# Optimization experiments

Hardware: AMD Instinct MI355X
Metric: run time of the kernel (lower is better)

The kernel has to match this reference:

```python
import jax, jax.numpy as jnp
import numpy as np

H = 16
D_MODEL = 1024
D_K = D_MODEL // H
MAX_REL = 16
REL_VOCAB = 2 * MAX_REL + 1


def _rel_pos_ids(seq_len):
    r = jnp.arange(seq_len)
    dist = r[None, :] - r[:, None]                      # [S,S]
    return jnp.clip(dist, -MAX_REL, MAX_REL) + MAX_REL  # in [0, 2*MAX_REL]


def setup_inputs() -> dict:
    key = jax.random.key(0)
    ks = jax.random.split(key, 16)
    B, S = 2, 2048
    f32 = jnp.float32
    inp = {
        "query": jax.random.normal(ks[0], (B, S, D_MODEL), f32),
        "key": jax.random.normal(ks[1], (B, S, D_MODEL), f32),
        "value": jax.random.normal(ks[2], (B, S, D_MODEL), f32),
        # four nn.Linear(d_model, d_model): W [out,in], b [out]
        "Wq": jax.random.normal(ks[3], (D_MODEL, D_MODEL), f32) * 0.02,
        "bq": jnp.zeros((D_MODEL,), f32),
        "Wk": jax.random.normal(ks[4], (D_MODEL, D_MODEL), f32) * 0.02,
        "bk": jnp.zeros((D_MODEL,), f32),
        "Wv": jax.random.normal(ks[5], (D_MODEL, D_MODEL), f32) * 0.02,
        "bv": jnp.zeros((D_MODEL,), f32),
        "Wo": jax.random.normal(ks[6], (D_MODEL, D_MODEL), f32) * 0.02,
        "bo": jnp.zeros((D_MODEL,), f32),
        # relative-position embedding tables (keys and values)
        "rel_k_table": jax.random.normal(ks[7], (REL_VOCAB, D_K), f32) * 0.02,
        "rel_v_table": jax.random.normal(ks[8], (REL_VOCAB, D_K), f32) * 0.02,
    }
    return inp


def reference(query, key, value, Wq, bq, Wk, bk, Wv, bv, Wo, bo,
              rel_k_table, rel_v_table):
    B, S, E = query.shape
    ids = _rel_pos_ids(S)                    # [S,S] int
    rel_k = rel_k_table[ids]                 # [S,S,d_k]
    rel_v = rel_v_table[ids]                 # [S,S,d_k]

    def proj(x, W, b):
        y = x @ W.T + b                      # [B,S,E]
        return y.reshape(B, S, H, D_K).transpose(0, 2, 1, 3)  # [B,H,S,d_k]

    q = proj(query, Wq, bq)
    k = proj(key, Wk, bk)
    v = proj(value, Wv, bv)

    # NOTE: original has no 1/sqrt(d_k) scaling and ignores mask — faithful.
    logits = jnp.einsum('bhqd,bhkd->bhqk', q, k) \
           + jnp.einsum('bhqd,qkd->bhqk', q, rel_k)
    w = jax.nn.softmax(logits, axis=-1)      # [B,H,S,S]

    x = jnp.einsum('bhqk,bhkd->bhqd', w, v) \
      + jnp.einsum('bhqk,qkd->bhqd', w, rel_v)

    x = x.transpose(0, 2, 1, 3).reshape(B, S, H * D_K)
    return x @ Wo.T + bo
```

## Files before the change

kernel.cpp:

```cpp
#include <hip/hip_runtime.h>
#include <hip/hip_bf16.h>

typedef unsigned short u16;
typedef __attribute__((ext_vector_type(8))) short short8;
typedef __attribute__((ext_vector_type(4))) short short4_t;
typedef __attribute__((ext_vector_type(4))) float f32x4;

#define MFMA16(a, b, c) __builtin_amdgcn_mfma_f32_16x16x32_bf16((a), (b), (c), 0, 0, 0)

#if __has_builtin(__builtin_amdgcn_mfma_f32_16x16x16bf16_1k)
#define MFMAK16(a, b, c) __builtin_amdgcn_mfma_f32_16x16x16bf16_1k((a), (b), (c), 0, 0, 0)
#elif __has_builtin(__builtin_amdgcn_mfma_f32_16x16x16_bf16)
#define MFMAK16(a, b, c) __builtin_amdgcn_mfma_f32_16x16x16_bf16((a), (b), (c), 0, 0, 0)
#else
__device__ __forceinline__ f32x4 mfmak16_asm(short4_t a, short4_t b, f32x4 c) {
  asm("v_mfma_f32_16x16x16_bf16 %0, %1, %2, %0" : "+v"(c) : "v"(a), "v"(b));
  return c;
}
#define MFMAK16(a, b, c) mfmak16_asm((a), (b), (c))
#endif

#define GLOAD_LDS16(gp, lp)                                          \
  __builtin_amdgcn_global_load_lds(                                  \
      (const __attribute__((address_space(1))) void*)(gp),           \
      (__attribute__((address_space(3))) void*)(lp), 16, 0, 0)
#define SBAR() asm volatile("s_barrier" ::: "memory")
#define WAIT_LGKM0() asm volatile("s_waitcnt lgkmcnt(0)" ::: "memory")
#define WAIT_VM0() asm volatile("s_waitcnt vmcnt(0)" ::: "memory")

__device__ __forceinline__ float us2f(u16 u) {
  union { unsigned int i; float f; } c; c.i = ((unsigned int)u) << 16; return c.f;
}
__device__ __forceinline__ u16 f2us(float f) {
  union { float f; unsigned int i; } c; c.f = f;
  return (u16)((c.i + 0x7fffu + ((c.i >> 16) & 1u)) >> 16);
}
__device__ __forceinline__ unsigned int f2us2(float a, float b) {
  union { __hip_bfloat162 h; unsigned int u; } c;
  c.h = __float22bfloat162_rn(float2{a, b});
  return c.u;
}

__global__ __launch_bounds__(256) void cvt_all_kernel(
    const float* x0, const float* x1, const float* x2, const float* w0,
    const float* w1, const float* w2, const float* w3, u16* y0, u16* y1,
    u16* y2, u16* z0, u16* z1, u16* z2, u16* z3) {
  const int z = blockIdx.z;
  const float* src; u16* dst; int n;
  switch (z) {
    case 0: src = x0; dst = y0; n = 4194304; break;
    case 1: src = x1; dst = y1; n = 4194304; break;
    case 2: src = x2; dst = y2; n = 4194304; break;
    case 3: src = w0; dst = z0; n = 1048576; break;
    case 4: src = w1; dst = z1; n = 1048576; break;
    case 5: src = w2; dst = z2; n = 1048576; break;
    default: src = w3; dst = z3; n = 1048576; break;
  }
  const int i = (blockIdx.x * 256 + threadIdx.x) * 8;
  if (i < n) {
    const float4 a = *(const float4*)(src + i);
    const float4 b = *(const float4*)(src + i + 4);
    unsigned int o[4];
    o[0] = f2us2(a.x, a.y); o[1] = f2us2(a.z, a.w);
    o[2] = f2us2(b.x, b.y); o[3] = f2us2(b.z, b.w);
    *(uint4*)(dst + i) = *(uint4*)o;
  }
}

__global__ __launch_bounds__(256) void cvt_relk_kernel(const float* relk, u16* relkb) {
  const int i = blockIdx.x * 256 + threadIdx.x;
  if (i < 4096) relkb[i] = (i < 2112) ? f2us(relk[i]) : (u16)0;
}

template <int MODE, typename OUT>
__device__ __forceinline__ void gemm_body(u16* __restrict__ SM,
                                          const u16* __restrict__ X,
                                          const u16* __restrict__ W,
                                          const float* __restrict__ bias,
                                          OUT* __restrict__ Y, int row0, int col0) {
  u16* As = SM;
  u16* Bs = SM + 8192;
  const int tid = threadIdx.x;
  const int lane = tid & 63;
  const int wid = tid >> 6;
  const int wm = wid >> 1, wn = wid & 1;
  const int l15 = lane & 15, l16 = lane >> 4;
  const int lrow = lane >> 3;
  const int lchunk = (lane & 7) ^ lrow;

  f32x4 acc[4][4];
#pragma unroll
  for (int i = 0; i < 4; i++)
#pragma unroll
    for (int j = 0; j < 4; j++) acc[i][j] = (f32x4){0.f, 0.f, 0.f, 0.f};

  for (int k0 = 0; k0 < 1024; k0 += 64) {
#pragma unroll
    for (int i = 0; i < 4; i++) {
      const int rb = wid * 32 + i * 8;
      GLOAD_LDS16(X + (size_t)(row0 + rb + lrow) * 1024 + k0 + lchunk * 8, &As[rb * 64]);
      GLOAD_LDS16(W + (size_t)(col0 + rb + lrow) * 1024 + k0 + lchunk * 8, &Bs[rb * 64]);
    }
    __syncthreads();
#pragma unroll
    for (int kk = 0; kk < 2; kk++) {
      const int ch = kk * 4 + l16;
      short8 af[4], bfr[4];
#pragma unroll
      for (int t = 0; t < 4; t++) {
        const int m = wm * 64 + t * 16 + l15;
        af[t] = *(const short8*)&As[m * 64 + ((ch ^ (m & 7)) * 8)];
        const int n = wn * 64 + t * 16 + l15;
        bfr[t] = *(const short8*)&Bs[n * 64 + ((ch ^ (n & 7)) * 8)];
      }
#pragma unroll
      for (int tm = 0; tm < 4; tm++)
#pragma unroll
        for (int tn = 0; tn < 4; tn++)
          acc[tm][tn] = MFMA16(af[tm], bfr[tn], acc[tm][tn]);
    }
    __syncthreads();
  }

  if (MODE == 0) {
#pragma unroll
    for (int tn = 0; tn < 4; tn++) {
      const int col = col0 + wn * 64 + tn * 16 + l15;
      const float bv = bias[col];
#pragma unroll
      for (int tm = 0; tm < 4; tm++) {
        const int rowb = row0 + wm * 64 + tm * 16 + l16 * 4;
#pragma unroll
        for (int r = 0; r < 4; r++)
          Y[(size_t)(rowb + r) * 1024 + col] = (OUT)(acc[tm][tn][r] + bv);
      }
    }
  } else {
    u16* T = SM;
    const int bb = row0 >> 11;
    const int sbase = row0 & 2047;
#pragma unroll
    for (int pass = 0; pass < 2; pass++) {
      __syncthreads();
      if (wm == pass) {
#pragma unroll
        for (int tn = 0; tn < 4; tn++) {
          const int coll = wn * 64 + tn * 16 + l15;
          const float bv = bias[col0 + coll];
#pragma unroll
          for (int tm = 0; tm < 4; tm++) {
            if (MODE == 1) {
#pragma unroll
              for (int r = 0; r < 4; r++)
                T[(tm * 16 + l16 * 4 + r) * 136 + coll] = f2us(acc[tm][tn][r] + bv);
            } else {
              unsigned int o[2];
              o[0] = f2us2(acc[tm][tn][0] + bv, acc[tm][tn][1] + bv);
              o[1] = f2us2(acc[tm][tn][2] + bv, acc[tm][tn][3] + bv);
              *(short4_t*)&T[coll * 72 + tm * 16 + l16 * 4] = *(short4_t*)o;
            }
          }
        }
      }
      __syncthreads();
      if (MODE == 1) {
#pragma unroll
        for (int i = 0; i < 8; i++) {
          const int idx = tid + i * 256;
          const int srow = idx >> 5, c4 = idx & 31;
          const short4_t v = *(const short4_t*)&T[srow * 136 + c4 * 4];
          const int col = col0 + c4 * 4;
          const int hh = col >> 6, dd = col & 63;
          const int s = sbase + pass * 64 + srow;
          *(short4_t*)&((u16*)Y)[(((size_t)(bb * 16 + hh)) * 2048 + s) * 64 + dd] = v;
        }
      } else {
#pragma unroll
        for (int i = 0; i < 4; i++) {
          const int idx = tid + i * 256;
          const int cl = idx >> 3, sc = idx & 7;
          const short8 v = *(const short8*)&T[cl * 72 + sc * 8];
          const int col = col0 + cl;
          const int hh = col >> 6, dd = col & 63;
          const int s = sbase + pass * 64 + sc * 8;
          *(short8*)&((u16*)Y)[(((size_t)(bb * 16 + hh)) * 64 + dd) * 2048 + s] = v;
        }
      }
    }
  }
}

__global__ __launch_bounds__(256) void qkv_kernel(
    const u16* Xq, const u16* Xk, const u16* Xv, const u16* Wq, const u16* Wk,
    const u16* Wv, const float* bq, const float* bk, const float* bv, u16* Yq,
    u16* Yk, u16* Yv) {
  __shared__ __align__(16) u16 SM[16384];
  const int z = blockIdx.z;
  const u16* X = z == 0 ? Xq : (z == 1 ? Xk : Xv);
  const u16* W = z == 0 ? Wq : (z == 1 ? Wk : Wv);
  const float* bi = z == 0 ? bq : (z == 1 ? bk : bv);
  u16* Y = z == 0 ? Yq : (z == 1 ? Yk : Yv);
  if (z == 2)
    gemm_body<2, u16>(SM, X, W, bi, Y, blockIdx.x * 128, blockIdx.y * 128);
  else
    gemm_body<1, u16>(SM, X, W, bi, Y, blockIdx.x * 128, blockIdx.y * 128);
}

__global__ __launch_bounds__(256) void oproj_kernel(const u16* Xc, const u16* Wo,
                                                    const float* bo, float* out) {
  __shared__ __align__(16) u16 SM[16384];
  gemm_body<0, float>(SM, Xc, Wo, bo, out, blockIdx.x * 128, blockIdx.y * 128);
}

__global__ __launch_bounds__(256, 6) void attn_kernel(
    const u16* __restrict__ Qg, const u16* __restrict__ Kg,
    const u16* __restrict__ Vtg, const u16* __restrict__ relkb,
    const float* __restrict__ relv, u16* __restrict__ ctx) {
  __shared__ __align__(16) u16 KV[8192];
  __shared__ __align__(16) u16 qrelJ[64 * 33];
  __shared__ __align__(16) u16 wsum[64 * 31];

  const int tid = threadIdx.x, lane = tid & 63, wid = tid >> 6;
  const int l15 = lane & 15, l16 = lane >> 4;
  const int bh = blockIdx.x;
  const int b = bh >> 4, h = bh & 15;
  const int q0 = blockIdx.y * 64;
  const u16* Qb = Qg + (size_t)bh * 2048 * 64;
  const u16* Kb = Kg + (size_t)bh * 2048 * 64;
  const u16* Vtb = Vtg + (size_t)bh * 64 * 2048;

  const int lrow = lane >> 3;
  const int lchunk = (lane & 7) ^ lrow;
  const int qw = wid * 16;
  const int kq4 = l16 * 4;
  const int qrow = qw + l15;

#pragma unroll
  for (int i = 0; i < 2; i++) {
    const int rb = wid * 16 + i * 8;
    GLOAD_LDS16(Qb + (size_t)(q0 + rb + lrow) * 64 + lchunk * 8, &KV[rb * 64]);
  }
  for (int idx = tid; idx < 992; idx += 256) ((unsigned int*)wsum)[idx] = 0u;
  __syncthreads();

  short8 aq[2];
  {
    const int m = qw + l15;
    aq[0] = *(const short8*)&KV[m * 64 + ((l16 ^ (m & 7)) * 8)];
    aq[1] = *(const short8*)&KV[m * 64 + (((4 + l16) ^ (m & 7)) * 8)];
  }
  {
    f32x4 qa[3];
#pragma unroll
    for (int nt = 0; nt < 3; nt++) {
      qa[nt] = (f32x4){0.f, 0.f, 0.f, 0.f};
#pragma unroll
      for (int kk = 0; kk < 2; kk++) {
        const short8 bf =
            *(const short8*)(relkb + (nt * 16 + l15) * 64 + kk * 32 + l16 * 8);
        qa[nt] = MFMA16(aq[kk], bf, qa[nt]);
      }
    }
#pragma unroll
    for (int nt = 0; nt < 3; nt++) {
      if (nt < 2 || l15 == 0) {
#pragma unroll
        for (int r = 0; r < 4; r++)
          qrelJ[(qw + kq4 + r) * 33 + nt * 16 + l15] = f2us(qa[nt][r]);
      }
    }
  }
  WAIT_LGKM0();
  const float q0r = us2f(qrelJ[qrow * 33 + 0]);
  const float q32r = us2f(qrelJ[qrow * 33 + 32]);

  float l_acc = 0.f, wl_acc = 0.f, wr_acc = 0.f;
  f32x4 Oacc[4];
#pragma unroll
  for (int t = 0; t < 4; t++) Oacc[t] = (f32x4){0.f, 0.f, 0.f, 0.f};

  for (int kt = 0; kt < 32; kt++) {
    SBAR();
    const int k0 = kt * 64;
#pragma unroll
    for (int i = 0; i < 2; i++) {
      const int rb = wid * 16 + i * 8;
      GLOAD_LDS16(Kb + (size_t)(k0 + rb + lrow) * 64 + lchunk * 8, &KV[rb * 64]);
    }
#pragma unroll
    for (int i = 0; i < 2; i++) {
      const int rb = wid * 16 + i * 8;
      GLOAD_LDS16(Vtb + (size_t)(rb + lrow) * 2048 + k0 + lchunk * 8,
                  &KV[4096 + rb * 64]);
    }
    WAIT_VM0();
    SBAR();

    short4_t pf[4];
    if (k0 + 79 <= q0 || k0 >= q0 + 79) {
      const float eb = (k0 < q0) ? q0r : q32r;
      float ts = 0.f;
#pragma unroll
      for (int tn = 0; tn < 4; tn++) {
        f32x4 sac = (f32x4){0.f, 0.f, 0.f, 0.f};
#pragma unroll
        for (int kk = 0; kk < 2; kk++) {
          const int n = tn * 16 + l15;
          const short8 bk = *(const short8*)&KV[n * 64 + (((kk * 4 + l16) ^ (n & 7)) * 8)];
          sac = MFMA16(bk, aq[kk], sac);
        }
        float p0 = __expf(sac[0] + eb), p1 = __expf(sac[1] + eb);
        float p2 = __expf(sac[2] + eb), p3 = __expf(sac[3] + eb);
        ts += (p0 + p1) + (p2 + p3);
        union { unsigned int u[2]; short4_t s; } c;
        c.u[0] = f2us2(p0, p1);
        c.u[1] = f2us2(p2, p3);
        pf[tn] = c.s;
      }
      l_acc += ts;
      if (k0 < q0) wl_acc += ts; else wr_acc += ts;
    } else {
#pragma unroll
      for (int tn = 0; tn < 4; tn++) {
        f32x4 sac = (f32x4){0.f, 0.f, 0.f, 0.f};
#pragma unroll
        for (int kk = 0; kk < 2; kk++) {
          const int n = tn * 16 + l15;
          const short8 bk = *(const short8*)&KV[n * 64 + (((kk * 4 + l16) ^ (n & 7)) * 8)];
          sac = MFMA16(bk, aq[kk], sac);
        }
        float pv4[4];
#pragma unroll
        for (int r = 0; r < 4; r++) {
          const int kg = k0 + tn * 16 + kq4 + r;
          const int dlt = kg - (q0 + qrow);
          const int jj = (dlt < -16 ? -16 : (dlt > 16 ? 16 : dlt)) + 16;
          const float pv = __expf(sac[r] + us2f(qrelJ[qrow * 33 + jj]));
          pv4[r] = pv;
          l_acc += pv;
          if (dlt <= -16) wl_acc += pv;
          else if (dlt >= 16) wr_acc += pv;
          else wsum[qrow * 31 + (dlt + 15)] = f2us(pv);
        }
        union { unsigned int u[2]; short4_t s; } c;
        c.u[0] = f2us2(pv4[0], pv4[1]);
        c.u[1] = f2us2(pv4[2], pv4[3]);
        pf[tn] = c.s;
      }
    }

#pragma unroll
    for (int td = 0; td < 4; td++) {
      const int row = td * 16 + l15;
      const int rs = row & 7;
#pragma unroll
      for (int kk = 0; kk < 4; kk++) {
        const short4_t vf = *(const short4_t*)&KV[4096 + row * 64 +
                                                  (((kk * 2 + (l16 >> 1)) ^ rs) * 8) +
                                                  (l16 & 1) * 4];
        Oacc[td] = MFMAK16(vf, pf[kk], Oacc[td]);
      }
    }
  }

  l_acc += __shfl_xor(l_acc, 16); l_acc += __shfl_xor(l_acc, 32);
  wl_acc += __shfl_xor(wl_acc, 16); wl_acc += __shfl_xor(wl_acc, 32);
  wr_acc += __shfl_xor(wr_acc, 16); wr_acc += __shfl_xor(wr_acc, 32);
  const float linv = 1.f / l_acc;
  wl_acc *= linv; wr_acc *= linv;

#pragma unroll
  for (int td = 0; td < 4; td++) {
    const f32x4 rv0 = *(const f32x4*)&relv[td * 16 + kq4];
    const f32x4 rv32 = *(const f32x4*)&relv[32 * 64 + td * 16 + kq4];
#pragma unroll
    for (int r = 0; r < 4; r++)
      Oacc[td][r] = Oacc[td][r] * linv + wl_acc * rv0[r] + wr_acc * rv32[r];
  }
  WAIT_LGKM0();
  for (int j = 1; j <= 31; j++) {
    const float wv = us2f(wsum[qrow * 31 + (j - 1)]) * linv;
#pragma unroll
    for (int td = 0; td < 4; td++) {
      const f32x4 rv = *(const f32x4*)&relv[j * 64 + td * 16 + kq4];
#pragma unroll
      for (int r = 0; r < 4; r++) Oacc[td][r] += wv * rv[r];
    }
  }
  SBAR();
#pragma unroll
  for (int td = 0; td < 4; td++) {
    unsigned int o[2];
    o[0] = f2us2(Oacc[td][0], Oacc[td][1]);
    o[1] = f2us2(Oacc[td][2], Oacc[td][3]);
    *(short4_t*)&KV[qrow * 72 + td * 16 + kq4] = *(short4_t*)o;
  }
  WAIT_LGKM0();
  SBAR();
#pragma unroll
  for (int i = 0; i < 2; i++) {
    const int idx = tid + i * 256;
    const int q = idx >> 3, sc = idx & 7;
    const short8 v = *(const short8*)&KV[q * 72 + sc * 8];
    *(short8*)&ctx[((size_t)b * 2048 + q0 + q) * 1024 + h * 64 + sc * 8] = v;
  }
}

extern "C" void kernel_launch(void* const* d_in, const int* in_sizes, int n_in,
                              void* d_out, int out_size, void* d_ws, size_t ws_size,
                              hipStream_t stream) {
  u16* qb = (u16*)d_ws;
  u16* kb = qb + 4194304;
  u16* vtb = kb + 4194304;
  u16* ctx = vtb + 4194304;
  u16* Xq = ctx + 4194304;
  u16* Xk = Xq + 4194304;
  u16* Xv = Xk + 4194304;
  u16* Wqb = Xv + 4194304;
  u16* Wkb = Wqb + 1048576;
  u16* Wvb = Wkb + 1048576;
  u16* Wob = Wvb + 1048576;
  u16* relkb = Wob + 1048576;

  const float* bq = (const float*)d_in[4];
  const float* bk = (const float*)d_in[6];
  const float* bv = (const float*)d_in[8];
  const float* bo = (const float*)d_in[10];
  const float* relk = (const float*)d_in[11];
  const float* relv = (const float*)d_in[12];

  dim3 blk(256);
  cvt_all_kernel<<<dim3(2048, 1, 7), blk, 0, stream>>>(
      (const float*)d_in[0], (const float*)d_in[1], (const float*)d_in[2],
      (const float*)d_in[3], (const float*)d_in[5], (const float*)d_in[7],
      (const float*)d_in[9], Xq, Xk, Xv, Wqb, Wkb, Wvb, Wob);
  cvt_relk_kernel<<<16, blk, 0, stream>>>(relk, relkb);
  qkv_kernel<<<dim3(32, 8, 3), blk, 0, stream>>>(Xq, Xk, Xv, Wqb, Wkb, Wvb, bq,
                                                 bk, bv, qb, kb, vtb);
  attn_kernel<<<dim3(32, 32), blk, 0, stream>>>(qb, kb, vtb, relkb, relv, ctx);
  oproj_kernel<<<dim3(32, 8), blk, 0, stream>>>(ctx, Wob, bo, (float*)d_out);
}
```

Baseline: 269.2 us.

## Double-buffer K/V tiles in attention and switch softmax to exp2

The attention kernel now double-buffers K and V^T tiles in LDS. It prefetches the next key tile with async global-to-LDS loads while computing on the current one, and uses partial vmcnt waits instead of a full drain every iteration. Q is pre-scaled by log2(e) in the QKV projection epilogue, so the softmax can use the hardware exp2 instruction; the relative-key logits are built from this scaled Q, so they stay consistent. The separate relk conversion kernel is merged into the bulk conversion kernel to save a launch, and s_setprio is raised around the PV MFMA block. In exchange, LDS use doubles and the launch-bounds occupancy hint drops from 6 to 4 blocks per CU.

```diff
diff --git a/kernel.cpp b/kernel.cpp
--- a/kernel.cpp
+++ b/kernel.cpp
@@ -27,6 +27,9 @@
 #define SBAR() asm volatile("s_barrier" ::: "memory")
 #define WAIT_LGKM0() asm volatile("s_waitcnt lgkmcnt(0)" ::: "memory")
 #define WAIT_VM0() asm volatile("s_waitcnt vmcnt(0)" ::: "memory")
+#define WAIT_VM4() asm volatile("s_waitcnt vmcnt(4)" ::: "memory")
+
+#define LOG2E 1.44269504088896340736f
 
 __device__ __forceinline__ float us2f(u16 u) {
   union { unsigned int i; float f; } c; c.i = ((unsigned int)u) << 16; return c.f;
@@ -40,12 +43,37 @@
   c.h = __float22bfloat162_rn(float2{a, b});
   return c.u;
 }
+__device__ __forceinline__ float exp2fast(float x) {
+#if __has_builtin(__builtin_amdgcn_exp2f)
+  return __builtin_amdgcn_exp2f(x);
+#else
+  return exp2f(x);
+#endif
+}
 
 __global__ __launch_bounds__(256) void cvt_all_kernel(
     const float* x0, const float* x1, const float* x2, const float* w0,
-    const float* w1, const float* w2, const float* w3, u16* y0, u16* y1,
-    u16* y2, u16* z0, u16* z1, u16* z2, u16* z3) {
+    const float* w1, const float* w2, const float* w3, const float* relk,
+    u16* y0, u16* y1, u16* y2, u16* z0, u16* z1, u16* z2, u16* z3,
+    u16* relkb) {
   const int z = blockIdx.z;
+  if (z == 7) {
+    const int i = (blockIdx.x * 256 + threadIdx.x) * 8;
+    if (i < 4096) {
+      if (i < 2112) {
+        const float4 a = *(const float4*)(relk + i);
+        const float4 b = *(const float4*)(relk + i + 4);
+        unsigned int o[4];
+        o[0] = f2us2(a.x, a.y); o[1] = f2us2(a.z, a.w);
+        o[2] = f2us2(b.x, b.y); o[3] = f2us2(b.z, b.w);
+        *(uint4*)(relkb + i) = *(uint4*)o;
+      } else {
+        uint4 zz = {0u, 0u, 0u, 0u};
+        *(uint4*)(relkb + i) = zz;
+      }
+    }
+    return;
+  }
   const float* src; u16* dst; int n;
   switch (z) {
     case 0: src = x0; dst = y0; n = 4194304; break;
@@ -67,17 +95,13 @@
   }
 }
 
-__global__ __launch_bounds__(256) void cvt_relk_kernel(const float* relk, u16* relkb) {
-  const int i = blockIdx.x * 256 + threadIdx.x;
-  if (i < 4096) relkb[i] = (i < 2112) ? f2us(relk[i]) : (u16)0;
-}
-
 template <int MODE, typename OUT>
 __device__ __forceinline__ void gemm_body(u16* __restrict__ SM,
                                           const u16* __restrict__ X,
                                           const u16* __restrict__ W,
                                           const float* __restrict__ bias,
-                                          OUT* __restrict__ Y, int row0, int col0) {
+                                          OUT* __restrict__ Y, int row0, int col0,
+                                          float oscale) {
   u16* As = SM;
   u16* Bs = SM + 8192;
   const int tid = threadIdx.x;
@@ -152,7 +176,7 @@
             if (MODE == 1) {
 #pragma unroll
               for (int r = 0; r < 4; r++)
-                T[(tm * 16 + l16 * 4 + r) * 136 + coll] = f2us(acc[tm][tn][r] + bv);
+                T[(tm * 16 + l16 * 4 + r) * 136 + coll] = f2us((acc[tm][tn][r] + bv) * oscale);
             } else {
               unsigned int o[2];
               o[0] = f2us2(acc[tm][tn][0] + bv, acc[tm][tn][1] + bv);
@@ -201,22 +225,23 @@
   const float* bi = z == 0 ? bq : (z == 1 ? bk : bv);
   u16* Y = z == 0 ? Yq : (z == 1 ? Yk : Yv);
   if (z == 2)
-    gemm_body<2, u16>(SM, X, W, bi, Y, blockIdx.x * 128, blockIdx.y * 128);
+    gemm_body<2, u16>(SM, X, W, bi, Y, blockIdx.x * 128, blockIdx.y * 128, 1.0f);
   else
-    gemm_body<1, u16>(SM, X, W, bi, Y, blockIdx.x * 128, blockIdx.y * 128);
+    gemm_body<1, u16>(SM, X, W, bi, Y, blockIdx.x * 128, blockIdx.y * 128,
+                      z == 0 ? LOG2E : 1.0f);
 }
 
 __global__ __launch_bounds__(256) void oproj_kernel(const u16* Xc, const u16* Wo,
                                                     const float* bo, float* out) {
   __shared__ __align__(16) u16 SM[16384];
-  gemm_body<0, float>(SM, Xc, Wo, bo, out, blockIdx.x * 128, blockIdx.y * 128);
-}
-
-__global__ __launch_bounds__(256, 6) void attn_kernel(
+  gemm_body<0, float>(SM, Xc, Wo, bo, out, blockIdx.x * 128, blockIdx.y * 128, 1.0f);
+}
+
+__global__ __launch_bounds__(256, 4) void attn_kernel(
     const u16* __restrict__ Qg, const u16* __restrict__ Kg,
     const u16* __restrict__ Vtg, const u16* __restrict__ relkb,
     const float* __restrict__ relv, u16* __restrict__ ctx) {
-  __shared__ __align__(16) u16 KV[8192];
+  __shared__ __align__(16) u16 KV[16384];
   __shared__ __align__(16) u16 qrelJ[64 * 33];
   __shared__ __align__(16) u16 wsum[64 * 31];
 
@@ -237,11 +262,22 @@
 
 #pragma unroll
   for (int i = 0; i < 2; i++) {
-    const int rb = wid * 16 + i * 8;
+    const int rb = qw + i * 8;
     GLOAD_LDS16(Qb + (size_t)(q0 + rb + lrow) * 64 + lchunk * 8, &KV[rb * 64]);
   }
+#pragma unroll
+  for (int i = 0; i < 2; i++) {
+    const int rb = qw + i * 8;
+    GLOAD_LDS16(Kb + (size_t)(rb + lrow) * 64 + lchunk * 8, &KV[8192 + rb * 64]);
+  }
+#pragma unroll
+  for (int i = 0; i < 2; i++) {
+    const int rb = qw + i * 8;
+    GLOAD_LDS16(Vtb + (size_t)(rb + lrow) * 2048 + lchunk * 8, &KV[12288 + rb * 64]);
+  }
   for (int idx = tid; idx < 992; idx += 256) ((unsigned int*)wsum)[idx] = 0u;
-  __syncthreads();
+  WAIT_VM4();
+  SBAR();
 
   short8 aq[2];
   {
@@ -273,6 +309,7 @@
   WAIT_LGKM0();
   const float q0r = us2f(qrelJ[qrow * 33 + 0]);
   const float q32r = us2f(qrelJ[qrow * 33 + 32]);
+  SBAR();
 
   float l_acc = 0.f, wl_acc = 0.f, wr_acc = 0.f;
   f32x4 Oacc[4];
@@ -280,21 +317,30 @@
   for (int t = 0; t < 4; t++) Oacc[t] = (f32x4){0.f, 0.f, 0.f, 0.f};
 
   for (int kt = 0; kt < 32; kt++) {
+    const int curb = (kt & 1) ? 0 : 8192;
+    const int k0 = kt * 64;
+    if (kt < 31) {
+      const int sb = curb ^ 8192;
+      const int k1 = k0 + 64;
+#pragma unroll
+      for (int i = 0; i < 2; i++) {
+        const int rb = qw + i * 8;
+        GLOAD_LDS16(Kb + (size_t)(k1 + rb + lrow) * 64 + lchunk * 8, &KV[sb + rb * 64]);
+      }
+#pragma unroll
+      for (int i = 0; i < 2; i++) {
+        const int rb = qw + i * 8;
+        GLOAD_LDS16(Vtb + (size_t)(rb + lrow) * 2048 + k1 + lchunk * 8,
+                    &KV[sb + 4096 + rb * 64]);
+      }
+      WAIT_VM4();
+    } else {
+      WAIT_VM0();
+    }
     SBAR();
-    const int k0 = kt * 64;
-#pragma unroll
-    for (int i = 0; i < 2; i++) {
-      const int rb = wid * 16 + i * 8;
-      GLOAD_LDS16(Kb + (size_t)(k0 + rb + lrow) * 64 + lchunk * 8, &KV[rb * 64]);
-    }
-#pragma unroll
-    for (int i = 0; i < 2; i++) {
-      const int rb = wid * 16 + i * 8;
-      GLOAD_LDS16(Vtb + (size_t)(rb + lrow) * 2048 + k0 + lchunk * 8,
-                  &KV[4096 + rb * 64]);
-    }
-    WAIT_VM0();
-    SBAR();
+
+    const u16* __restrict__ Ks = &KV[curb];
+    const u16* __restrict__ Vs = &KV[curb + 4096];
 
     short4_t pf[4];
     if (k0 + 79 <= q0 || k0 >= q0 + 79) {
@@ -306,11 +352,11 @@
 #pragma unroll
         for (int kk = 0; kk < 2; kk++) {
           const int n = tn * 16 + l15;
-          const short8 bk = *(const short8*)&KV[n * 64 + (((kk * 4 + l16) ^ (n & 7)) * 8)];
+          const short8 bk = *(const short8*)&Ks[n * 64 + (((kk * 4 + l16) ^ (n & 7)) * 8)];
           sac = MFMA16(bk, aq[kk], sac);
         }
-        float p0 = __expf(sac[0] + eb), p1 = __expf(sac[1] + eb);
-        float p2 = __expf(sac[2] + eb), p3 = __expf(sac[3] + eb);
+        float p0 = exp2fast(sac[0] + eb), p1 = exp2fast(sac[1] + eb);
+        float p2 = exp2fast(sac[2] + eb), p3 = exp2fast(sac[3] + eb);
         ts += (p0 + p1) + (p2 + p3);
         union { unsigned int u[2]; short4_t s; } c;
         c.u[0] = f2us2(p0, p1);
@@ -326,7 +372,7 @@
 #pragma unroll
         for (int kk = 0; kk < 2; kk++) {
           const int n = tn * 16 + l15;
-          const short8 bk = *(const short8*)&KV[n * 64 + (((kk * 4 + l16) ^ (n & 7)) * 8)];
+          const short8 bk = *(const short8*)&Ks[n * 64 + (((kk * 4 + l16) ^ (n & 7)) * 8)];
           sac = MFMA16(bk, aq[kk], sac);
         }
         float pv4[4];
@@ -335,7 +381,7 @@
           const int kg = k0 + tn * 16 + kq4 + r;
           const int dlt = kg - (q0 + qrow);
           const int jj = (dlt < -16 ? -16 : (dlt > 16 ? 16 : dlt)) + 16;
-          const float pv = __expf(sac[r] + us2f(qrelJ[qrow * 33 + jj]));
+          const float pv = exp2fast(sac[r] + us2f(qrelJ[qrow * 33 + jj]));
           pv4[r] = pv;
           l_acc += pv;
           if (dlt <= -16) wl_acc += pv;
@@ -349,18 +395,22 @@
       }
     }
 
+    __builtin_amdgcn_s_setprio(1);
 #pragma unroll
     for (int td = 0; td < 4; td++) {
       const int row = td * 16 + l15;
       const int rs = row & 7;
 #pragma unroll
       for (int kk = 0; kk < 4; kk++) {
-        const short4_t vf = *(const short4_t*)&KV[4096 + row * 64 +
+        const short4_t vf = *(const short4_t*)&Vs[row * 64 +
                                                   (((kk * 2 + (l16 >> 1)) ^ rs) * 8) +
                                                   (l16 & 1) * 4];
         Oacc[td] = MFMAK16(vf, pf[kk], Oacc[td]);
       }
     }
+    __builtin_amdgcn_s_setprio(0);
+
+    SBAR();
   }
 
   l_acc += __shfl_xor(l_acc, 16); l_acc += __shfl_xor(l_acc, 32);
@@ -387,7 +437,6 @@
       for (int r = 0; r < 4; r++) Oacc[td][r] += wv * rv[r];
     }
   }
-  SBAR();
 #pragma unroll
   for (int td = 0; td < 4; td++) {
     unsigned int o[2];
@@ -430,11 +479,10 @@
   const float* relv = (const float*)d_in[12];
 
   dim3 blk(256);
-  cvt_all_kernel<<<dim3(2048, 1, 7), blk, 0, stream>>>(
+  cvt_all_kernel<<<dim3(2048, 1, 8), blk, 0, stream>>>(
       (const float*)d_in[0], (const float*)d_in[1], (const float*)d_in[2],
       (const float*)d_in[3], (const float*)d_in[5], (const float*)d_in[7],
-      (const float*)d_in[9], Xq, Xk, Xv, Wqb, Wkb, Wvb, Wob);
-  cvt_relk_kernel<<<16, blk, 0, stream>>>(relk, relkb);
+      (const float*)d_in[9], relk, Xq, Xk, Xv, Wqb, Wkb, Wvb, Wob, relkb);
   qkv_kernel<<<dim3(32, 8, 3), blk, 0, stream>>>(Xq, Xk, Xv, Wqb, Wkb, Wvb, bq,
                                                  bk, bv, qb, kb, vtb);
   attn_kernel<<<dim3(32, 32), blk, 0, stream>>>(qb, kb, vtb, relkb, relv, ctx);
```

Result: no change. 271.3 us (+0.8%).
